# Optimization experiments

Hardware: AMD Instinct MI355X
Metric: run time of the kernel (lower is better)

Reference implementation:

```python
import jax, jax.numpy as jnp
import numpy as np

BATCH, D, N = 16, 128, 16
E = N * (N - 1) // 2  # 120 candidate edges (strict upper triangle)


def _incidence(A, n):
    """Build edge-incidence matrices G, H of shape [b, n, E] from binary edge
    vector A [b, E] over the strict upper triangle of an n x n adjacency."""
    r, c = np.triu_indices(n, k=1)
    mask = (A > 0).astype(jnp.float32)  # [b, E]
    node = jnp.arange(n)[:, None]       # [n, 1]
    G = (node == jnp.asarray(r)[None, :]).astype(jnp.float32)[None] * mask[:, None, :]
    H = (node == jnp.asarray(c)[None, :]).astype(jnp.float32)[None] * mask[:, None, :]
    return G, H


def _kron(t1, t2):
    """Batched Kronecker product: t1 [b,r1,c1], t2 [b,r2,c2] -> [b,r1*r2,c1*c2]."""
    b, r1, c1 = t1.shape
    _, r2, c2 = t2.shape
    return (t1[:, :, None, :, None] * t2[:, None, :, None, :]).reshape(b, r1 * r2, c1 * c2)


def setup_inputs() -> dict:
    key = jax.random.key(0)
    ks = jax.random.split(key, 8)
    A_src = jax.random.randint(ks[0], (BATCH, E), 0, 2, dtype=jnp.int32)
    A_tgt = jax.random.randint(ks[1], (BATCH, E), 0, 2, dtype=jnp.int32)
    F_src = jax.random.normal(ks[2], (BATCH, D, N), dtype=jnp.float32)
    F_tgt = jax.random.normal(ks[3], (BATCH, D, N), dtype=jnp.float32)
    U_src = jax.random.normal(ks[4], (BATCH, N, N), dtype=jnp.float32)
    U_tgt = jax.random.normal(ks[5], (BATCH, N, N), dtype=jnp.float32)
    stdv = 1.0 / np.sqrt(D * 2)
    eye_half = jnp.eye(D, dtype=jnp.float32) / 2.0
    lambda1 = jax.random.uniform(ks[6], (D, D), jnp.float32, -stdv, stdv) + eye_half
    lambda2 = jax.random.uniform(ks[7], (D, D), jnp.float32, -stdv, stdv) + eye_half
    return {"A_src": A_src, "A_tgt": A_tgt, "F_src": F_src, "F_tgt": F_tgt,
            "U_src": U_src, "U_tgt": U_tgt, "lambda1": lambda1, "lambda2": lambda2}


def reference(A_src, A_tgt, F_src, F_tgt, U_src, U_tgt, lambda1, lambda2):
    b = F_src.shape[0]
    n, m = F_src.shape[-1], F_tgt.shape[-1]
    # symmetrized, relu'd block weight (w1 = w2 = 1)
    l1 = jax.nn.relu(lambda1 + lambda1.T)
    l2 = jax.nn.relu(lambda2 + lambda2.T)
    weight = jnp.block([[l1, l2], [l2, l1]])  # [2d, 2d]
    # incidence matrices (vectorized replacement of the per-batch scatter loop)
    G1, H1 = _incidence(A_src, n)  # [b, n, E]
    G2, H2 = _incidence(A_tgt, m)  # [b, m, E]
    # edge features: X = cat(F G, F H) -> [b, 2d, E]
    X = jnp.concatenate([F_src @ G1, F_src @ H1], axis=1)
    Y = jnp.concatenate([F_tgt @ G2, F_tgt @ H2], axis=1)
    # edge affinity M_e = X^T W Y : [b, E, E]
    M_e = jnp.einsum('bie,ij,bjf->bef', X, weight, Y)
    # node affinity M_p = U_src^T U_tgt : [b, n, m]
    M_p = jnp.einsum('bdn,bdm->bnm', U_src, U_tgt)
    K1 = _kron(G2, G1)  # [b, m*n, E*E]
    K2 = _kron(H2, H1)  # [b, m*n, E*E]
    # per-column scaling of K1 by flattened M_e (replaces per-column loop)
    K1_new = K1 * M_e.reshape(b, 1, -1)
    diagMp = jax.vmap(jnp.diag)(M_p.reshape(b, -1))  # [b, n*m, n*m]
    M = diagMp + jnp.einsum('bik,bjk->bij', K1_new, K2)
    return M
```

## Files before the change

kernel.cpp:

```cpp
#include <hip/hip_runtime.h>

#define NB 16
#define DD 128
#define NN 16
#define NE 120

__device__ __forceinline__ int edge_idx(int a, int p) {
    return (a * (31 - a)) / 2 + (p - a - 1);
}

__global__ __launch_bounds__(256) void kT(const float* __restrict__ Ftgt,
                                          const float* __restrict__ lam1,
                                          const float* __restrict__ lam2,
                                          float* __restrict__ ws) {
    __shared__ float sFt[DD * NN];
    int blk = blockIdx.x;
    int b = blk >> 4;
    int lsel = (blk >> 3) & 1;
    int islice = blk & 7;
    int t = threadIdx.x;

    const float* F = Ftgt + b * (DD * NN);
    for (int k = t; k < DD * NN; k += 256) sFt[k] = F[k];
    __syncthreads();

    const float* lam = lsel ? lam2 : lam1;
    int i = (islice << 4) | (t >> 4);
    int v = t & 15;

    float acc = 0.f;
#pragma unroll 4
    for (int j = 0; j < DD; ++j) {
        float w = lam[i * DD + j] + lam[j * DD + i];
        w = fmaxf(w, 0.f);
        acc = fmaf(w, sFt[(j << 4) | v], acc);
    }
    ws[(((b * 2 + lsel) * DD) + i) * NN + v] = acc;
}

__global__ __launch_bounds__(256) void kP(const float* __restrict__ Fsrc,
                                          const float* __restrict__ Usrc,
                                          const float* __restrict__ Utgt,
                                          float* __restrict__ ws) {
    __shared__ float sFs[DD * NN];
    __shared__ float sT1[DD * NN];
    __shared__ float sT2[DD * NN];
    int b = blockIdx.x;
    int t = threadIdx.x;

    const float* F = Fsrc + b * (DD * NN);
    const float* T1 = ws + ((b * 2 + 0) * DD) * NN;
    const float* T2 = ws + ((b * 2 + 1) * DD) * NN;
    for (int k = t; k < DD * NN; k += 256) {
        sFs[k] = F[k];
        sT1[k] = T1[k];
        sT2[k] = T2[k];
    }
    __syncthreads();

    int u = t >> 4;
    int v = t & 15;

    float p1 = 0.f, p2 = 0.f;
#pragma unroll 4
    for (int i = 0; i < DD; ++i) {
        float fs = sFs[(i << 4) | u];
        p1 = fmaf(fs, sT1[(i << 4) | v], p1);
        p2 = fmaf(fs, sT2[(i << 4) | v], p2);
    }

    const float* Us = Usrc + b * (NN * NN);
    const float* Ut = Utgt + b * (NN * NN);
    float mp = 0.f;
#pragma unroll
    for (int d = 0; d < NN; ++d)
        mp = fmaf(Us[(d << 4) | u], Ut[(d << 4) | v], mp);

    float* out = ws + 65536 + b * 768;
    out[t] = p1;
    out[t + 256] = p2;
    out[t + 512] = mp;
}

__global__ __launch_bounds__(256) void kC(const int* __restrict__ Asrc,
                                          const int* __restrict__ Atgt,
                                          const float* __restrict__ ws,
                                          float* __restrict__ out) {
    __shared__ float sP1[256];
    __shared__ float sP2[256];
    __shared__ float sMp[256];
    __shared__ int smask[128];

    int blk = blockIdx.x;
    int b = blk >> 6;
    int t = threadIdx.x;

    const float* tab = ws + 65536 + b * 768;
    sP1[t] = tab[t];
    sP2[t] = tab[t + 256];
    sMp[t] = tab[t + 512];
    if (t < NE) smask[t] = (Asrc[b * NE + t] > 0) && (Atgt[b * NE + t] > 0);
    __syncthreads();

    int r = ((blk & 63) << 2) | (t >> 6);
    int j0 = (t & 63) << 2;
    int a = r >> 4, c = r & 15, p = j0 >> 4;

    bool condT = (a < p) && (smask[edge_idx(a, p)] != 0);
    float cpart = sP1[(a << 4) | c] + sP2[(p << 4) | c];

    float4 vec;
    float* vv = (float*)&vec;
#pragma unroll
    for (int s = 0; s < 4; ++s) {
        int j = j0 + s;
        int q = j & 15;
        float x = 0.f;
        if (condT && (c < q) && (smask[edge_idx(c, q)] != 0))
            x = cpart + sP2[(a << 4) | q] + sP1[(p << 4) | q];
        if (r == j) x += sMp[r];
        vv[s] = x;
    }
    *(float4*)(out + ((size_t)b << 16) + (r << 8) + j0) = vec;
}

extern "C" void kernel_launch(void* const* d_in, const int* in_sizes, int n_in,
                              void* d_out, int out_size, void* d_ws, size_t ws_size,
                              hipStream_t stream) {
    const int*   A_src  = (const int*)d_in[0];
    const int*   A_tgt  = (const int*)d_in[1];
    const float* F_src  = (const float*)d_in[2];
    const float* F_tgt  = (const float*)d_in[3];
    const float* U_src  = (const float*)d_in[4];
    const float* U_tgt  = (const float*)d_in[5];
    const float* lam1   = (const float*)d_in[6];
    const float* lam2   = (const float*)d_in[7];
    float* out = (float*)d_out;
    float* ws  = (float*)d_ws;

    kT<<<256, 256, 0, stream>>>(F_tgt, lam1, lam2, ws);
    kP<<<16, 256, 0, stream>>>(F_src, U_src, U_tgt, ws);
    kC<<<1024, 256, 0, stream>>>(A_src, A_tgt, ws, out);
}
```

Before: 87.14 us.

## Fuse three kernels into one per-batch kernel with redundant T computation

Replaces the three-launch pipeline (T = W·Ft, P tables, output fill) with a single kernel of 32 blocks, two per batch element. Each block recomputes the full T1/T2 products for its batch in shared memory, using a transposed lambda tile and 16-wide register accumulation, then writes half of the 256x256 output. This removes two launch gaps and the workspace round-trips. In exchange it uses only 32 blocks instead of 1024 for the output write, and duplicates the T matmul in both blocks of each batch.

New measurement: 128.2 us. +47.1%, slower.

```diff
diff --git a/kernel.cpp b/kernel.cpp
--- a/kernel.cpp
+++ b/kernel.cpp
@@ -1,144 +1,157 @@
 #include <hip/hip_runtime.h>
 
-#define NB 16
-#define DD 128
-#define NN 16
-#define NE 120
 
 __device__ __forceinline__ int edge_idx(int a, int p) {
     return (a * (31 - a)) / 2 + (p - a - 1);
 }
 
-__global__ __launch_bounds__(256) void kT(const float* __restrict__ Ftgt,
-                                          const float* __restrict__ lam1,
-                                          const float* __restrict__ lam2,
-                                          float* __restrict__ ws) {
-    __shared__ float sFt[DD * NN];
-    int blk = blockIdx.x;
-    int b = blk >> 4;
-    int lsel = (blk >> 3) & 1;
-    int islice = blk & 7;
-    int t = threadIdx.x;
+#define LTS 130
+#define TS  17
 
-    const float* F = Ftgt + b * (DD * NN);
-    for (int k = t; k < DD * NN; k += 256) sFt[k] = F[k];
-    __syncthreads();
+__global__ __launch_bounds__(256) void kAll(
+    const int* __restrict__ Asrc, const int* __restrict__ Atgt,
+    const float* __restrict__ Fsrc, const float* __restrict__ Ftgt,
+    const float* __restrict__ Usrc, const float* __restrict__ Utgt,
+    const float* __restrict__ lam1, const float* __restrict__ lam2,
+    float* __restrict__ out)
+{
+    __shared__ float sFt[2048];
+    __shared__ float sFs[2048];
+    __shared__ float sLT[16 * LTS];
+    __shared__ float sTp[128 * TS];
+    __shared__ float sT1[128 * TS];
+    __shared__ float sT2[128 * TS];
+    __shared__ float sP1[16 * TS];
+    __shared__ float sP2[16 * TS];
+    __shared__ float sMp[256];
+    __shared__ int   smask[120];
 
-    const float* lam = lsel ? lam2 : lam1;
-    int i = (islice << 4) | (t >> 4);
-    int v = t & 15;
+    const int blk  = blockIdx.x;
+    const int b    = blk >> 1;
+    const int half = blk & 1;
+    const int t    = threadIdx.x;
 
-    float acc = 0.f;
-#pragma unroll 4
-    for (int j = 0; j < DD; ++j) {
-        float w = lam[i * DD + j] + lam[j * DD + i];
-        w = fmaxf(w, 0.f);
-        acc = fmaf(w, sFt[(j << 4) | v], acc);
-    }
-    ws[(((b * 2 + lsel) * DD) + i) * NN + v] = acc;
-}
+    const float* Ft = Ftgt + b * 2048;
+    const float* Fs = Fsrc + b * 2048;
+    for (int k = t; k < 2048; k += 256) { sFt[k] = Ft[k]; sFs[k] = Fs[k]; }
+    if (t < 120) smask[t] = (Asrc[b * 120 + t] > 0) && (Atgt[b * 120 + t] > 0);
 
-__global__ __launch_bounds__(256) void kP(const float* __restrict__ Fsrc,
-                                          const float* __restrict__ Usrc,
-                                          const float* __restrict__ Utgt,
-                                          float* __restrict__ ws) {
-    __shared__ float sFs[DD * NN];
-    __shared__ float sT1[DD * NN];
-    __shared__ float sT2[DD * NN];
-    int b = blockIdx.x;
-    int t = threadIdx.x;
+    const int i = t & 127;
+    const int h = t >> 7;
 
-    const float* F = Fsrc + b * (DD * NN);
-    const float* T1 = ws + ((b * 2 + 0) * DD) * NN;
-    const float* T2 = ws + ((b * 2 + 1) * DD) * NN;
-    for (int k = t; k < DD * NN; k += 256) {
-        sFs[k] = F[k];
-        sT1[k] = T1[k];
-        sT2[k] = T2[k];
+    for (int lsel = 0; lsel < 2; ++lsel) {
+        const float* lam = lsel ? lam2 : lam1;
+        float acc[16];
+#pragma unroll
+        for (int v = 0; v < 16; ++v) acc[v] = 0.f;
+
+        for (int j0 = 0; j0 < 128; j0 += 16) {
+            __syncthreads();
+#pragma unroll
+            for (int it = 0; it < 8; ++it) {
+                const int k = t + it * 256;
+                sLT[(k & 15) * LTS + (k >> 4)] = lam[(k >> 4) * 128 + j0 + (k & 15)];
+            }
+            __syncthreads();
+#pragma unroll
+            for (int jj = 0; jj < 8; ++jj) {
+                const int jl = h * 8 + jj;
+                const int j  = j0 + jl;
+                float w = sLT[jl * LTS + i] + lam[j * 128 + i];
+                w = fmaxf(w, 0.f);
+                const float4* fr = (const float4*)(sFt + (j << 4));
+                const float4 f0 = fr[0], f1 = fr[1], f2 = fr[2], f3 = fr[3];
+                acc[0]  = fmaf(w, f0.x, acc[0]);
+                acc[1]  = fmaf(w, f0.y, acc[1]);
+                acc[2]  = fmaf(w, f0.z, acc[2]);
+                acc[3]  = fmaf(w, f0.w, acc[3]);
+                acc[4]  = fmaf(w, f1.x, acc[4]);
+                acc[5]  = fmaf(w, f1.y, acc[5]);
+                acc[6]  = fmaf(w, f1.z, acc[6]);
+                acc[7]  = fmaf(w, f1.w, acc[7]);
+                acc[8]  = fmaf(w, f2.x, acc[8]);
+                acc[9]  = fmaf(w, f2.y, acc[9]);
+                acc[10] = fmaf(w, f2.z, acc[10]);
+                acc[11] = fmaf(w, f2.w, acc[11]);
+                acc[12] = fmaf(w, f3.x, acc[12]);
+                acc[13] = fmaf(w, f3.y, acc[13]);
+                acc[14] = fmaf(w, f3.z, acc[14]);
+                acc[15] = fmaf(w, f3.w, acc[15]);
+            }
+        }
+        __syncthreads();
+        if (h == 1) {
+#pragma unroll
+            for (int v = 0; v < 16; ++v) sTp[i * TS + v] = acc[v];
+        }
+        __syncthreads();
+        float* sT = lsel ? sT2 : sT1;
+        if (h == 0) {
+#pragma unroll
+            for (int v = 0; v < 16; ++v) sT[i * TS + v] = acc[v] + sTp[i * TS + v];
+        }
     }
     __syncthreads();
 
-    int u = t >> 4;
-    int v = t & 15;
-
-    float p1 = 0.f, p2 = 0.f;
-#pragma unroll 4
-    for (int i = 0; i < DD; ++i) {
-        float fs = sFs[(i << 4) | u];
-        p1 = fmaf(fs, sT1[(i << 4) | v], p1);
-        p2 = fmaf(fs, sT2[(i << 4) | v], p2);
+    {
+        const int u = t >> 4, v = t & 15;
+        float p1 = 0.f, p2 = 0.f;
+#pragma unroll 8
+        for (int d = 0; d < 128; ++d) {
+            const float fs = sFs[(d << 4) | u];
+            p1 = fmaf(fs, sT1[d * TS + v], p1);
+            p2 = fmaf(fs, sT2[d * TS + v], p2);
+        }
+        const float* Us = Usrc + b * 256;
+        const float* Ut = Utgt + b * 256;
+        float mp = 0.f;
+#pragma unroll
+        for (int d = 0; d < 16; ++d)
+            mp = fmaf(Us[(d << 4) | u], Ut[(d << 4) | v], mp);
+        sP1[u * TS + v] = p1;
+        sP2[u * TS + v] = p2;
+        sMp[t] = mp;
     }
-
-    const float* Us = Usrc + b * (NN * NN);
-    const float* Ut = Utgt + b * (NN * NN);
-    float mp = 0.f;
-#pragma unroll
-    for (int d = 0; d < NN; ++d)
-        mp = fmaf(Us[(d << 4) | u], Ut[(d << 4) | v], mp);
-
-    float* out = ws + 65536 + b * 768;
-    out[t] = p1;
-    out[t + 256] = p2;
-    out[t + 512] = mp;
-}
-
-__global__ __launch_bounds__(256) void kC(const int* __restrict__ Asrc,
-                                          const int* __restrict__ Atgt,
-                                          const float* __restrict__ ws,
-                                          float* __restrict__ out) {
-    __shared__ float sP1[256];
-    __shared__ float sP2[256];
-    __shared__ float sMp[256];
-    __shared__ int smask[128];
-
-    int blk = blockIdx.x;
-    int b = blk >> 6;
-    int t = threadIdx.x;
-
-    const float* tab = ws + 65536 + b * 768;
-    sP1[t] = tab[t];
-    sP2[t] = tab[t + 256];
-    sMp[t] = tab[t + 512];
-    if (t < NE) smask[t] = (Asrc[b * NE + t] > 0) && (Atgt[b * NE + t] > 0);
     __syncthreads();
 
-    int r = ((blk & 63) << 2) | (t >> 6);
-    int j0 = (t & 63) << 2;
-    int a = r >> 4, c = r & 15, p = j0 >> 4;
-
-    bool condT = (a < p) && (smask[edge_idx(a, p)] != 0);
-    float cpart = sP1[(a << 4) | c] + sP2[(p << 4) | c];
-
-    float4 vec;
-    float* vv = (float*)&vec;
+    const int rbase = (half << 7) + (t >> 6);
+    const int j0c   = (t & 63) << 2;
+    const int p     = j0c >> 4;
+    float* outB = out + ((size_t)b << 16);
+#pragma unroll 4
+    for (int rr = 0; rr < 32; ++rr) {
+        const int r = rbase + (rr << 2);
+        const int a = r >> 4, c = r & 15;
+        const bool condT = (a < p) && (smask[edge_idx(a, p)] != 0);
+        const float cpart = sP1[a * TS + c] + sP2[p * TS + c];
+        float4 vec;
+        float* vv = (float*)&vec;
 #pragma unroll
-    for (int s = 0; s < 4; ++s) {
-        int j = j0 + s;
-        int q = j & 15;
-        float x = 0.f;
-        if (condT && (c < q) && (smask[edge_idx(c, q)] != 0))
-            x = cpart + sP2[(a << 4) | q] + sP1[(p << 4) | q];
-        if (r == j) x += sMp[r];
-        vv[s] = x;
+        for (int s = 0; s < 4; ++s) {
+            const int j = j0c + s, q = j & 15;
+            float x = 0.f;
+            if (condT && (c < q) && (smask[edge_idx(c, q)] != 0))
+                x = cpart + sP2[a * TS + q] + sP1[p * TS + q];
+            if (r == j) x += sMp[r];
+            vv[s] = x;
+        }
+        *(float4*)(outB + (r << 8) + j0c) = vec;
     }
-    *(float4*)(out + ((size_t)b << 16) + (r << 8) + j0) = vec;
 }
 
 extern "C" void kernel_launch(void* const* d_in, const int* in_sizes, int n_in,
                               void* d_out, int out_size, void* d_ws, size_t ws_size,
                               hipStream_t stream) {
-    const int*   A_src  = (const int*)d_in[0];
-    const int*   A_tgt  = (const int*)d_in[1];
-    const float* F_src  = (const float*)d_in[2];
-    const float* F_tgt  = (const float*)d_in[3];
-    const float* U_src  = (const float*)d_in[4];
-    const float* U_tgt  = (const float*)d_in[5];
-    const float* lam1   = (const float*)d_in[6];
-    const float* lam2   = (const float*)d_in[7];
+    const int*   A_src = (const int*)d_in[0];
+    const int*   A_tgt = (const int*)d_in[1];
+    const float* F_src = (const float*)d_in[2];
+    const float* F_tgt = (const float*)d_in[3];
+    const float* U_src = (const float*)d_in[4];
+    const float* U_tgt = (const float*)d_in[5];
+    const float* lam1  = (const float*)d_in[6];
+    const float* lam2  = (const float*)d_in[7];
     float* out = (float*)d_out;
-    float* ws  = (float*)d_ws;
 
-    kT<<<256, 256, 0, stream>>>(F_tgt, lam1, lam2, ws);
-    kP<<<16, 256, 0, stream>>>(F_src, U_src, U_tgt, ws);
-    kC<<<1024, 256, 0, stream>>>(A_src, A_tgt, ws, out);
+    kAll<<<32, 256, 0, stream>>>(A_src, A_tgt, F_src, F_tgt,
+                                 U_src, U_tgt, lam1, lam2, out);
 }
```
